# Optimization experiments

Hardware: AMD Instinct MI355X
Metric: run time of the kernel (lower is better)

The kernel has to match this reference:

```python
import jax, jax.numpy as jnp
import numpy as np

T, G = 8, 128                      # time frames, spatial grid per axis
RMIN, RMAX = -1.5, 1.5             # same range for x, y, z
STEP = (RMAX - RMIN) / G           # voxel step per axis
# corner order: [C000, C100, C010, C110, C001, C101, C011, C111]
_OFFSETS = jnp.array([[0,0,0],[1,0,0],[0,1,0],[1,1,0],
                      [0,0,1],[1,0,1],[0,1,1],[1,1,1]], dtype=jnp.int32)

def _trilinear_coef(p):
    # p: [N,3] fractional position inside the cell, in [0,1)
    u, v, w = p[:, 0], p[:, 1], p[:, 2]
    return jnp.stack([(1-u)*(1-v)*(1-w), u*(1-v)*(1-w), (1-u)*v*(1-w), u*v*(1-w),
                      (1-u)*(1-v)*w,     u*(1-v)*w,     (1-u)*v*w,     u*v*w], axis=1)

def setup_inputs() -> dict:
    key = jax.random.key(0)
    k1, k2, k3, k4 = jax.random.split(key, 4)
    N = 1048576
    pos = jax.random.uniform(k1, (N, 3), jnp.float32, RMIN, RMAX)
    t = jax.random.randint(k2, (N,), 0, T, dtype=jnp.int32)
    sigma = jax.random.uniform(k3, (N,), jnp.float32)
    target_norm = jax.random.normal(k4, (N, 3), jnp.float32)
    lr = jnp.full((1,), 0.1, jnp.float32)
    voxel_array = jnp.full((T, G, G, G, 3), jnp.sqrt(1.0 / 3.0), jnp.float32)
    return {"t": t, "pos": pos, "lr": lr, "sigma": sigma,
            "target_norm": target_norm, "voxel_array": voxel_array}

def reference(t, pos, lr, sigma, target_norm, voxel_array):
    # shift into [0, range) coords (all axes share the same range/step)
    pos_s = pos - RMIN
    min_idx = jnp.floor(pos_s / STEP).astype(jnp.int32)          # [N,3], == // in source
    idx = jnp.clip(min_idx[:, None, :] + _OFFSETS[None], 0, G - 1)  # [N,8,3]
    frac = jnp.mod(pos_s, STEP) / STEP                           # [N,3]
    coef = _trilinear_coef(frac)                                 # [N,8]
    xi, yi, zi = idx[..., 0], idx[..., 1], idx[..., 2]
    ti = jnp.broadcast_to(t[:, None], xi.shape)                  # [N,8]
    vertex_values = voxel_array[ti, xi, yi, zi]                  # [N,8,3] gather
    value = jnp.sum(coef[:, :, None] * vertex_values, axis=1)    # [N,3]
    # update weights
    sigma_weight = (1.0 - jnp.exp(-sigma))[:, None]              # [N,1]
    update_lambda = jax.nn.sigmoid(lr * sigma_weight * coef)[..., None]  # [N,8,1]
    new_vertex_values = update_lambda * target_norm[:, None, :] + (1.0 - update_lambda) * vertex_values
    diff = new_vertex_values - vertex_values                     # [N,8,3]
    new_voxel = voxel_array.at[ti.reshape(-1), xi.reshape(-1),
                               yi.reshape(-1), zi.reshape(-1)].add(diff.reshape(-1, 3))
    return value, new_voxel
```

## Files before the change

kernel.cpp:

```cpp
#include <hip/hip_runtime.h>
#include <hip/hip_fp16.h>
#include <math.h>


#define GRES 128
#define NBINS (8 * 128 * 128)
#define CAP 16
#define OVF_MAX 16384
#define SCAN_BLOCKS 512
constexpr float RMIN_F = -1.5f;
constexpr float STEP_F = 3.0f / 128.0f;

typedef float f32x4a4 __attribute__((ext_vector_type(4), aligned(4)));
typedef float f32x2a4 __attribute__((ext_vector_type(2), aligned(4)));

__device__ __forceinline__ float fast_sigmoid(float x) {
    if (__builtin_expect(fabsf(x) < 0.5f, 1)) {
        return fmaf(x, fmaf(x * x, -(1.0f / 48.0f), 0.25f), 0.5f);
    }
    return 1.0f / (1.0f + __expf(-x));
}

__device__ __forceinline__ uint4 make_payload(
    int i, float px, float py, float pz, int mz,
    const float* __restrict__ target, float lrsw)
{
    float u = fmodf(px, STEP_F) / STEP_F;
    float v = fmodf(py, STEP_F) / STEP_F;
    float w = fmodf(pz, STEP_F) / STEP_F;
    unsigned qu = (unsigned)(u * 2047.0f + 0.5f);
    unsigned qv = (unsigned)(v * 2047.0f + 0.5f);
    unsigned qw = (unsigned)(w * 1023.0f + 0.5f);
    unsigned hx = (unsigned)__half_as_ushort(__float2half(target[3 * i + 0]));
    unsigned hy = (unsigned)__half_as_ushort(__float2half(target[3 * i + 1]));
    unsigned hz = (unsigned)__half_as_ushort(__float2half(target[3 * i + 2]));
    unsigned hl = (unsigned)__half_as_ushort(__float2half(lrsw));
    uint4 p;
    p.x = (qu << 21) | (qv << 10) | qw;
    p.y = ((unsigned)i << 7) | (unsigned)mz;
    p.z = hx | (hy << 16);
    p.w = hz | (hl << 16);
    return p;
}

__global__ __launch_bounds__(256) void place_kernel(
    const int*   __restrict__ t,     const float* __restrict__ pos,
    const float* __restrict__ lr_p,  const float* __restrict__ sigma,
    const float* __restrict__ target,
    unsigned* __restrict__ hist,     uint4* __restrict__ bins,
    unsigned* __restrict__ ovfcnt,   unsigned* __restrict__ ovf_key,
    uint4*    __restrict__ ovf_pay,  int N)
{
    int i = blockIdx.x * blockDim.x + threadIdx.x;
    if (i >= N) return;
    float px = pos[3 * i + 0] - RMIN_F;
    float py = pos[3 * i + 1] - RMIN_F;
    float pz = pos[3 * i + 2] - RMIN_F;
    int cx = min((int)floorf(px / STEP_F), GRES - 1);
    int cy = min((int)floorf(py / STEP_F), GRES - 1);
    int mz = min((int)floorf(pz / STEP_F), GRES - 1);
    float lrsw = lr_p[0] * (1.0f - __expf(-sigma[i]));
    uint4 p = make_payload(i, px, py, pz, mz, target, lrsw);
    unsigned key  = ((unsigned)t[i] << 14) | ((unsigned)cx << 7) | (unsigned)cy;
    unsigned rank = atomicAdd(&hist[key], 1u);
    if (rank < CAP) {
        bins[(size_t)key * CAP + rank] = p;
    } else {
        unsigned o = atomicAdd(ovfcnt, 1u);
        if (o < OVF_MAX) { ovf_key[o] = key; ovf_pay[o] = p; }
    }
}

__global__ __launch_bounds__(256) void key_hist_kernel(
    const int* __restrict__ t, const float* __restrict__ pos,
    unsigned* __restrict__ keys, unsigned* __restrict__ hist, int N)
{
    int i = blockIdx.x * blockDim.x + threadIdx.x;
    if (i >= N) return;
    float px = pos[3 * i + 0] - RMIN_F;
    float py = pos[3 * i + 1] - RMIN_F;
    int cx = min((int)floorf(px / STEP_F), GRES - 1);
    int cy = min((int)floorf(py / STEP_F), GRES - 1);
    unsigned key  = ((unsigned)t[i] << 14) | ((unsigned)cx << 7) | (unsigned)cy;
    unsigned rank = atomicAdd(&hist[key], 1u);
    keys[i] = (key << 15) | rank;
}

__global__ __launch_bounds__(256) void scanA_kernel(
    const unsigned* __restrict__ hist, unsigned* __restrict__ binstart,
    unsigned* __restrict__ partial)
{
    __shared__ unsigned sh[256];
    const int tid = threadIdx.x;
    const int gid = blockIdx.x * 256 + tid;
    unsigned x = hist[gid];
    sh[tid] = x;
    __syncthreads();
    for (int off = 1; off < 256; off <<= 1) {
        unsigned v = (tid >= off) ? sh[tid - off] : 0u;
        __syncthreads();
        sh[tid] += v;
        __syncthreads();
    }
    binstart[gid] = sh[tid] - x;
    if (tid == 255) partial[blockIdx.x] = sh[255];
}

__global__ __launch_bounds__(256) void scanC_kernel(
    unsigned* __restrict__ binstart, const unsigned* __restrict__ partial, int N)
{
    __shared__ unsigned s_w[4];
    unsigned loc = 0;
    for (int i = threadIdx.x; i < blockIdx.x; i += 256) loc += partial[i];
    #pragma unroll
    for (int off = 32; off > 0; off >>= 1) loc += __shfl_down(loc, off);
    if ((threadIdx.x & 63) == 0) s_w[threadIdx.x >> 6] = loc;
    __syncthreads();
    const unsigned off0 = s_w[0] + s_w[1] + s_w[2] + s_w[3];
    const int gid = blockIdx.x * 256 + threadIdx.x;
    binstart[gid] += off0;
    if (gid == 0) binstart[NBINS] = (unsigned)N;
}

__global__ __launch_bounds__(256) void scatter_kernel(
    const float* __restrict__ pos, const float* __restrict__ lr_p,
    const float* __restrict__ sigma, const float* __restrict__ target,
    const unsigned* __restrict__ keys, const unsigned* __restrict__ binstart,
    uint4* __restrict__ sorted, int N)
{
    int i = blockIdx.x * blockDim.x + threadIdx.x;
    if (i >= N) return;
    unsigned kr   = keys[i];
    unsigned key  = kr >> 15;
    unsigned rank = kr & 0x7fffu;
    unsigned slot = binstart[key] + rank;
    float px = pos[3 * i + 0] - RMIN_F;
    float py = pos[3 * i + 1] - RMIN_F;
    float pz = pos[3 * i + 2] - RMIN_F;
    int   mz = min((int)floorf(pz / STEP_F), GRES - 1);
    float lrsw = lr_p[0] * (1.0f - __expf(-sigma[i]));
    sorted[slot] = make_payload(i, px, py, pz, mz, target, lrsw);
}

__device__ __forceinline__ void process_event(
    const uint4 p, const int cx, const int cy,
    const int x0, const int y0, const size_t tbase,
    const float* __restrict__ voxel_in,
    float* __restrict__ out_value, float* __restrict__ s_acc)
{
    const float u = (float)(p.x >> 21)           * (1.0f / 2047.0f);
    const float v = (float)((p.x >> 10) & 2047u) * (1.0f / 2047.0f);
    const float w = (float)(p.x & 1023u)         * (1.0f / 1023.0f);
    const int  mz  = (int)(p.y & 127u);
    const int  idx = (int)(p.y >> 7);
    const float tx = __half2float(__ushort_as_half((unsigned short)(p.z & 0xffffu)));
    const float ty = __half2float(__ushort_as_half((unsigned short)(p.z >> 16)));
    const float tz = __half2float(__ushort_as_half((unsigned short)(p.w & 0xffffu)));
    const float lrsw = __half2float(__ushort_as_half((unsigned short)(p.w >> 16)));

    const int xs1 = min(cx + 1, GRES - 1);
    const int ys1 = min(cy + 1, GRES - 1);
    const int zs1 = min(mz + 1, GRES - 1);
    const int zb  = min(mz, GRES - 2);
    const bool ztop = (mz == GRES - 1);

    float lo[4][3], hi[4][3];
    #pragma unroll
    for (int q = 0; q < 4; ++q) {
        const int xi = (q & 1) ? xs1 : cx;
        const int yi = (q & 2) ? ys1 : cy;
        const float* vp = voxel_in + tbase + (((size_t)xi * GRES + yi) * GRES + zb) * 3;
        f32x4a4 f0 = *(const f32x4a4*)vp;
        f32x2a4 f1 = *(const f32x2a4*)(vp + 4);
        hi[q][0] = f0.w; hi[q][1] = f1.x; hi[q][2] = f1.y;
        lo[q][0] = ztop ? f0.w : f0.x;
        lo[q][1] = ztop ? f1.x : f0.y;
        lo[q][2] = ztop ? f1.y : f0.z;
    }

    float c[8];
    c[0] = (1.f - u) * (1.f - v) * (1.f - w);
    c[1] =        u  * (1.f - v) * (1.f - w);
    c[2] = (1.f - u) *        v  * (1.f - w);
    c[3] =        u  *        v  * (1.f - w);
    c[4] = (1.f - u) * (1.f - v) *        w;
    c[5] =        u  * (1.f - v) *        w;
    c[6] = (1.f - u) *        v  *        w;
    c[7] =        u  *        v  *        w;

    const bool owner = (cx >= x0) && (cy >= y0);

    float vx = 0.f, vy = 0.f, vz = 0.f;
    #pragma unroll
    for (int q = 0; q < 4; ++q) {
        if (owner) {
            vx += c[q] * lo[q][0] + c[q + 4] * hi[q][0];
            vy += c[q] * lo[q][1] + c[q + 4] * hi[q][1];
            vz += c[q] * lo[q][2] + c[q + 4] * hi[q][2];
        }
        const int xi = (q & 1) ? xs1 : cx;
        const int yi = (q & 2) ? ys1 : cy;
        const int sxi = xi - x0, syi = yi - y0;
        if (sxi >= 0 && sxi < 4 && syi >= 0 && syi < 4) {
            const int col = ((sxi * 4 + syi) * 128) * 3;
            const float laml = fast_sigmoid(lrsw * c[q]);
            const int sal = col + mz * 3;
            atomicAdd(&s_acc[sal + 0], laml * (tx - lo[q][0]));
            atomicAdd(&s_acc[sal + 1], laml * (ty - lo[q][1]));
            atomicAdd(&s_acc[sal + 2], laml * (tz - lo[q][2]));
            const float lamh = fast_sigmoid(lrsw * c[q + 4]);
            const int sah = col + zs1 * 3;
            atomicAdd(&s_acc[sah + 0], lamh * (tx - hi[q][0]));
            atomicAdd(&s_acc[sah + 1], lamh * (ty - hi[q][1]));
            atomicAdd(&s_acc[sah + 2], lamh * (tz - hi[q][2]));
        }
    }
    if (owner) {
        out_value[3 * idx + 0] = vx;
        out_value[3 * idx + 1] = vy;
        out_value[3 * idx + 2] = vz;
    }
}

__global__ __launch_bounds__(256, 6) void brick_kernel(
    const unsigned* __restrict__ counts,
    const uint4*    __restrict__ sorted,
    const float*    __restrict__ voxel_in,
    float*          __restrict__ out_value,
    float*          __restrict__ out_voxel,
    int cap,
    const unsigned* __restrict__ ovf_key,
    const uint4*    __restrict__ ovf_pay,
    const unsigned* __restrict__ ovfcnt)
{
    __shared__ __align__(16) float s_acc[4 * 4 * 128 * 3];
    __shared__ unsigned s_start[25];
    __shared__ unsigned s_pref[26];
    __shared__ unsigned s_novf;

    const int vb = ((blockIdx.x & 7) << 10) | (blockIdx.x >> 3);
    const int t  = vb >> 10;
    const int bx = (vb >> 5) & 31;
    const int by = vb & 31;
    const int x0 = bx << 2, y0 = by << 2;
    const int tid = threadIdx.x;
    const size_t tbase = (size_t)t * (GRES * GRES * GRES * 3);

    float4* s_acc4 = (float4*)s_acc;
    for (int q = tid; q < 16 * 96; q += 256) s_acc4[q] = make_float4(0.f, 0.f, 0.f, 0.f);

    if (tid < 64) {
        unsigned st = 0, cnt = 0;
        if (tid < 25) {
            int dxb = tid / 5 - 1, dyb = tid % 5 - 1;
            int cx = x0 + dxb, cy = y0 + dyb;
            if (cx >= 0 && cx < GRES && cy >= 0 && cy < GRES) {
                unsigned key = ((unsigned)t << 14) | ((unsigned)cx << 7) | (unsigned)cy;
                if (cap > 0) {
                    st  = key * (unsigned)cap;
                    cnt = min(counts[key], (unsigned)cap);
                } else {
                    st  = counts[key];
                    cnt = counts[key + 1] - st;
                }
            }
            s_start[tid] = st;
        }
        unsigned x = cnt;
        #pragma unroll
        for (int off = 1; off < 32; off <<= 1) {
            unsigned y = __shfl_up(x, off);
            if (tid >= off) x += y;
        }
        if (tid < 25) s_pref[tid + 1] = x;
        if (tid == 0) s_pref[0] = 0;
    }
    if (tid == 64) s_novf = (cap > 0) ? *ovfcnt : 0u;
    __syncthreads();
    const int P = (int)s_pref[25];

    for (int j = tid; j < P; j += 256) {
        int b = 0;
        #pragma unroll
        for (int s = 16; s > 0; s >>= 1) {
            int nb = b + s;
            if (nb <= 24 && s_pref[nb] <= (unsigned)j) b = nb;
        }
        const int cx = x0 + b / 5 - 1, cy = y0 + b % 5 - 1;
        const unsigned g = s_start[b] + ((unsigned)j - s_pref[b]);
        process_event(sorted[g], cx, cy, x0, y0, tbase, voxel_in, out_value, s_acc);
    }

    if (cap > 0) {
        const unsigned novf = min(s_novf, (unsigned)OVF_MAX);
        for (unsigned o = tid; o < novf; o += 256) {
            const unsigned key = ovf_key[o];
            if ((int)(key >> 14) != t) continue;
            const int ocx = (int)((key >> 7) & 127u), ocy = (int)(key & 127u);
            const int dxb = ocx - x0, dyb = ocy - y0;
            if (dxb < -1 || dxb > 3 || dyb < -1 || dyb > 3) continue;
            process_event(ovf_pay[o], ocx, ocy, x0, y0, tbase, voxel_in, out_value, s_acc);
        }
    }
    __syncthreads();

    for (int q = tid; q < 16 * 96; q += 256) {
        int row = q / 96, r = q - row * 96;
        int ox = row >> 2, oy = row & 3;
        const size_t coff = tbase + (size_t)(x0 + ox) * 49152 + (size_t)(y0 + oy) * 384;
        float4 a = *((const float4*)(voxel_in + coff) + r);
        float4 d = s_acc4[q];
        *((float4*)(out_voxel + coff) + r) =
            make_float4(a.x + d.x, a.y + d.y, a.z + d.z, a.w + d.w);
    }
}

extern "C" void kernel_launch(void* const* d_in, const int* in_sizes, int n_in,
                              void* d_out, int out_size, void* d_ws, size_t ws_size,
                              hipStream_t stream) {
    const int*   t      = (const int*)  d_in[0];
    const float* pos    = (const float*)d_in[1];
    const float* lr     = (const float*)d_in[2];
    const float* sigma  = (const float*)d_in[3];
    const float* target = (const float*)d_in[4];
    const float* voxel  = (const float*)d_in[5];

    const int N = in_sizes[0];

    float* out_value = (float*)d_out;
    float* out_voxel = out_value + (size_t)3 * N;

    const int block = 256;
    const int grid  = (N + block - 1) / block;

    const size_t need = (size_t)NBINS * CAP * 16 + (size_t)NBINS * 4 + 64
                      + (size_t)OVF_MAX * 4 + (size_t)OVF_MAX * 16;

    if (ws_size >= need) {
        uint4*    bins    = (uint4*)d_ws;
        unsigned* hist    = (unsigned*)(bins + (size_t)NBINS * CAP);
        unsigned* ovfcnt  = hist + NBINS;
        unsigned* ovf_key = ovfcnt + 16;
        uint4*    ovf_pay = (uint4*)(ovf_key + OVF_MAX);

        hipMemsetAsync(hist, 0, NBINS * sizeof(unsigned) + 64, stream);
        place_kernel<<<grid, block, 0, stream>>>(t, pos, lr, sigma, target,
                                                 hist, bins, ovfcnt, ovf_key,
                                                 ovf_pay, N);
        brick_kernel<<<8192, 256, 0, stream>>>(hist, bins, voxel,
                                               out_value, out_voxel,
                                               CAP, ovf_key, ovf_pay, ovfcnt);
    } else {
        uint4*    sorted   = (uint4*)d_ws;
        unsigned* keys     = (unsigned*)(sorted + (size_t)N);
        unsigned* hist     = keys + N;
        unsigned* binstart = hist + NBINS;
        unsigned* partial  = binstart + (NBINS + 1);

        hipMemsetAsync(hist, 0, NBINS * sizeof(unsigned), stream);
        key_hist_kernel<<<grid, block, 0, stream>>>(t, pos, keys, hist, N);
        scanA_kernel<<<SCAN_BLOCKS, 256, 0, stream>>>(hist, binstart, partial);
        scanC_kernel<<<SCAN_BLOCKS, 256, 0, stream>>>(binstart, partial, N);
        scatter_kernel<<<grid, block, 0, stream>>>(pos, lr, sigma, target, keys,
                                                   binstart, sorted, N);
        brick_kernel<<<8192, 256, 0, stream>>>(binstart, sorted, voxel,
                                               out_value, out_voxel,
                                               0, nullptr, nullptr, nullptr);
    }
}
```

Baseline: 507.4 us.

## Split brick blocks into two z-halves with halved shared accumulator

Each brick block now covers only half the z range of its 4x4 xy column, so the grid doubles and the shared accumulator halves. Launch bounds rise from 6 to 8 blocks per CU to allow higher occupancy. Every block still reads all payloads of its 25 neighbouring bins but drops events whose z cell lies outside its half, with a one-cell halo at the boundary. In exchange, each payload is read twice across the two z-halves, and events at z=63 compute and write their output value twice.

```diff
diff --git a/kernel.cpp b/kernel.cpp
--- a/kernel.cpp
+++ b/kernel.cpp
@@ -144,7 +144,7 @@
 
 __device__ __forceinline__ void process_event(
     const uint4 p, const int cx, const int cy,
-    const int x0, const int y0, const size_t tbase,
+    const int x0, const int y0, const int z0, const size_t tbase,
     const float* __restrict__ voxel_in,
     float* __restrict__ out_value, float* __restrict__ s_acc)
 {
@@ -163,6 +163,8 @@
     const int zs1 = min(mz + 1, GRES - 1);
     const int zb  = min(mz, GRES - 2);
     const bool ztop = (mz == GRES - 1);
+    const int szl = mz  - z0;
+    const int szh = zs1 - z0;
 
     float lo[4][3], hi[4][3];
     #pragma unroll
@@ -202,17 +204,21 @@
         const int yi = (q & 2) ? ys1 : cy;
         const int sxi = xi - x0, syi = yi - y0;
         if (sxi >= 0 && sxi < 4 && syi >= 0 && syi < 4) {
-            const int col = ((sxi * 4 + syi) * 128) * 3;
-            const float laml = fast_sigmoid(lrsw * c[q]);
-            const int sal = col + mz * 3;
-            atomicAdd(&s_acc[sal + 0], laml * (tx - lo[q][0]));
-            atomicAdd(&s_acc[sal + 1], laml * (ty - lo[q][1]));
-            atomicAdd(&s_acc[sal + 2], laml * (tz - lo[q][2]));
-            const float lamh = fast_sigmoid(lrsw * c[q + 4]);
-            const int sah = col + zs1 * 3;
-            atomicAdd(&s_acc[sah + 0], lamh * (tx - hi[q][0]));
-            atomicAdd(&s_acc[sah + 1], lamh * (ty - hi[q][1]));
-            atomicAdd(&s_acc[sah + 2], lamh * (tz - hi[q][2]));
+            const int col = (sxi * 4 + syi) * 64;
+            if (szl >= 0 && szl < 64) {
+                const float laml = fast_sigmoid(lrsw * c[q]);
+                const int sal = (col + szl) * 3;
+                atomicAdd(&s_acc[sal + 0], laml * (tx - lo[q][0]));
+                atomicAdd(&s_acc[sal + 1], laml * (ty - lo[q][1]));
+                atomicAdd(&s_acc[sal + 2], laml * (tz - lo[q][2]));
+            }
+            if (szh >= 0 && szh < 64) {
+                const float lamh = fast_sigmoid(lrsw * c[q + 4]);
+                const int sah = (col + szh) * 3;
+                atomicAdd(&s_acc[sah + 0], lamh * (tx - hi[q][0]));
+                atomicAdd(&s_acc[sah + 1], lamh * (ty - hi[q][1]));
+                atomicAdd(&s_acc[sah + 2], lamh * (tz - hi[q][2]));
+            }
         }
     }
     if (owner) {
@@ -222,7 +228,7 @@
     }
 }
 
-__global__ __launch_bounds__(256, 6) void brick_kernel(
+__global__ __launch_bounds__(256, 8) void brick_kernel(
     const unsigned* __restrict__ counts,
     const uint4*    __restrict__ sorted,
     const float*    __restrict__ voxel_in,
@@ -233,21 +239,24 @@
     const uint4*    __restrict__ ovf_pay,
     const unsigned* __restrict__ ovfcnt)
 {
-    __shared__ __align__(16) float s_acc[4 * 4 * 128 * 3];
+    __shared__ __align__(16) float s_acc[4 * 4 * 64 * 3];
     __shared__ unsigned s_start[25];
     __shared__ unsigned s_pref[26];
     __shared__ unsigned s_novf;
 
-    const int vb = ((blockIdx.x & 7) << 10) | (blockIdx.x >> 3);
-    const int t  = vb >> 10;
-    const int bx = (vb >> 5) & 31;
-    const int by = vb & 31;
-    const int x0 = bx << 2, y0 = by << 2;
+    const int t  = blockIdx.x & 7;
+    const int s  = blockIdx.x >> 3;
+    const int bx = s >> 6;
+    const int by = (s >> 1) & 31;
+    const int zh = s & 1;
+    const int x0 = bx << 2, y0 = by << 2, z0 = zh << 6;
+    const int zlo = z0 ? z0 - 1 : 0;
+    const int zhi = z0 + 63;
     const int tid = threadIdx.x;
     const size_t tbase = (size_t)t * (GRES * GRES * GRES * 3);
 
     float4* s_acc4 = (float4*)s_acc;
-    for (int q = tid; q < 16 * 96; q += 256) s_acc4[q] = make_float4(0.f, 0.f, 0.f, 0.f);
+    for (int q = tid; q < 768; q += 256) s_acc4[q] = make_float4(0.f, 0.f, 0.f, 0.f);
 
     if (tid < 64) {
         unsigned st = 0, cnt = 0;
@@ -282,13 +291,16 @@
     for (int j = tid; j < P; j += 256) {
         int b = 0;
         #pragma unroll
-        for (int s = 16; s > 0; s >>= 1) {
-            int nb = b + s;
+        for (int sh = 16; sh > 0; sh >>= 1) {
+            int nb = b + sh;
             if (nb <= 24 && s_pref[nb] <= (unsigned)j) b = nb;
         }
         const int cx = x0 + b / 5 - 1, cy = y0 + b % 5 - 1;
         const unsigned g = s_start[b] + ((unsigned)j - s_pref[b]);
-        process_event(sorted[g], cx, cy, x0, y0, tbase, voxel_in, out_value, s_acc);
+        const uint4 p = sorted[g];
+        const int mz = (int)(p.y & 127u);
+        if (mz < zlo || mz > zhi) continue;
+        process_event(p, cx, cy, x0, y0, z0, tbase, voxel_in, out_value, s_acc);
     }
 
     if (cap > 0) {
@@ -299,15 +311,19 @@
             const int ocx = (int)((key >> 7) & 127u), ocy = (int)(key & 127u);
             const int dxb = ocx - x0, dyb = ocy - y0;
             if (dxb < -1 || dxb > 3 || dyb < -1 || dyb > 3) continue;
-            process_event(ovf_pay[o], ocx, ocy, x0, y0, tbase, voxel_in, out_value, s_acc);
+            const uint4 p = ovf_pay[o];
+            const int mz = (int)(p.y & 127u);
+            if (mz < zlo || mz > zhi) continue;
+            process_event(p, ocx, ocy, x0, y0, z0, tbase, voxel_in, out_value, s_acc);
         }
     }
     __syncthreads();
 
-    for (int q = tid; q < 16 * 96; q += 256) {
-        int row = q / 96, r = q - row * 96;
-        int ox = row >> 2, oy = row & 3;
-        const size_t coff = tbase + (size_t)(x0 + ox) * 49152 + (size_t)(y0 + oy) * 384;
+    for (int q = tid; q < 768; q += 256) {
+        int col = q / 48, r = q - col * 48;
+        int ox = col >> 2, oy = col & 3;
+        const size_t coff = tbase + (size_t)(x0 + ox) * 49152
+                                  + (size_t)(y0 + oy) * 384 + (size_t)z0 * 3;
         float4 a = *((const float4*)(voxel_in + coff) + r);
         float4 d = s_acc4[q];
         *((float4*)(out_voxel + coff) + r) =
@@ -347,9 +363,9 @@
         place_kernel<<<grid, block, 0, stream>>>(t, pos, lr, sigma, target,
                                                  hist, bins, ovfcnt, ovf_key,
                                                  ovf_pay, N);
-        brick_kernel<<<8192, 256, 0, stream>>>(hist, bins, voxel,
-                                               out_value, out_voxel,
-                                               CAP, ovf_key, ovf_pay, ovfcnt);
+        brick_kernel<<<16384, 256, 0, stream>>>(hist, bins, voxel,
+                                                out_value, out_voxel,
+                                                CAP, ovf_key, ovf_pay, ovfcnt);
     } else {
         uint4*    sorted   = (uint4*)d_ws;
         unsigned* keys     = (unsigned*)(sorted + (size_t)N);
@@ -363,8 +379,8 @@
         scanC_kernel<<<SCAN_BLOCKS, 256, 0, stream>>>(binstart, partial, N);
         scatter_kernel<<<grid, block, 0, stream>>>(pos, lr, sigma, target, keys,
                                                    binstart, sorted, N);
-        brick_kernel<<<8192, 256, 0, stream>>>(binstart, sorted, voxel,
-                                               out_value, out_voxel,
-                                               0, nullptr, nullptr, nullptr);
-    }
-}
+        brick_kernel<<<16384, 256, 0, stream>>>(binstart, sorted, voxel,
+                                                out_value, out_voxel,
+                                                0, nullptr, nullptr, nullptr);
+    }
+}
```

After: 510.1 us. No clear change (+0.5%).
